# Performance work log

Measured on AMD Instinct MI355X. Metric: run time of the kernel, lower is better.

Reference implementation:

```python
import jax, jax.numpy as jnp
import numpy as np

# Dimensions (match init_kwargs / input_specs)
B, C, H, W = 16, 96, 224, 224
COUT = 96
PH, PW = 16, 16          # patch_size (== patch_stride, non-overlapping)
KH, KW = 3, 3            # patch_kernel and output_kernel
PAD = 1                  # padding
GH, GW = H // PH, W // PW
P = GH * GW              # num_patches = 196


def setup_inputs() -> dict:
    key = jax.random.key(0)
    k1, k2, k3 = jax.random.split(key, 3)
    x = jax.random.normal(k1, (B, C, H, W), dtype=jnp.float32)
    # kaiming-normal-ish init scales (fan_in over trailing dims, as torch does)
    pf = jax.random.normal(k2, (C, P, 1, KH, KW), dtype=jnp.float32) * np.float32(np.sqrt(2.0 / (P * KH * KW)))
    of = jax.random.normal(k3, (COUT, C, KH, KW), dtype=jnp.float32) * np.float32(np.sqrt(2.0 / (C * KH * KW)))
    return {"x": x, "patch_filters": pf, "output_filters": of}


def _self_conv2d(x, patch_filters):
    """Locally-connected per-patch depthwise conv.

    x: (B, C, H, W); patch_filters: (C, P, 1, KH, KW).
    Each of the P non-overlapping PHxPW patches of each channel is convolved
    with its own KHxKW kernel (padding=PAD, stride=1), then patches are
    reassembled into the full (B, C, H, W) map.
    """
    # (B, C, GH, PH, GW, PW) -> (B, C, GH, GW, PH, PW) -> (B, C*P, PH, PW)
    xp = x.reshape(B, C, GH, PH, GW, PW).transpose(0, 1, 2, 4, 3, 5).reshape(B, C * P, PH, PW)
    k = patch_filters.reshape(C * P, 1, KH, KW)
    y = jax.lax.conv_general_dilated(
        xp, k,
        window_strides=(1, 1),
        padding=[(PAD, PAD), (PAD, PAD)],
        feature_group_count=C * P,
        dimension_numbers=("NCHW", "OIHW", "NCHW"),
    )  # (B, C*P, PH, PW) since 3x3 conv with pad 1 preserves size
    return y.reshape(B, C, GH, GW, PH, PW).transpose(0, 1, 2, 4, 3, 5).reshape(B, C, H, W)


def reference(x, patch_filters, output_filters):
    # input already at (max_input_height, max_input_width) -> F.pad is a no-op
    sa = _self_conv2d(x, patch_filters)
    out = jax.lax.conv_general_dilated(
        sa, output_filters,
        window_strides=(1, 1),
        padding=[(PAD, PAD), (PAD, PAD)],
        dimension_numbers=("NCHW", "OIHW", "NCHW"),
    )  # (B, COUT, H, W)
    return jax.nn.gelu(out, approximate=False)  # torch nn.GELU() = exact erf gelu
```

## Files before the change

### kernel.cpp

```cpp
#include <hip/hip_runtime.h>
#include <hip/hip_bf16.h>

#define B_    16
#define C_    96
#define H_    224
#define W_    224
#define COUT_ 96
#define GH_   14
#define GW_   14
#define P_    196
#define HW_   (H_*W_)
#define NCH_  12

#define AS1 __attribute__((address_space(1)))
#define AS3 __attribute__((address_space(3)))

typedef __attribute__((ext_vector_type(8))) unsigned short ushort8;
typedef __attribute__((ext_vector_type(8))) short        short8;
typedef __attribute__((ext_vector_type(4))) float        f32x4;

__device__ __forceinline__ unsigned short f2bf(float f) {
    union { __hip_bfloat16 h; unsigned short u; } cv;
    cv.h = __float2bfloat16(f);
    return cv.u;
}

__global__ __launch_bounds__(256) void prep_ofb(const float* __restrict__ of,
                                                unsigned short* __restrict__ ofb,
                                                unsigned short* __restrict__ zp) {
    if (blockIdx.x == 0 && threadIdx.x < 128) zp[threadIdx.x] = 0;
    int idx = blockIdx.x * 256 + threadIdx.x;
    if (idx < 9 * 96 * 96) {
        int tap = idx / (96 * 96);
        int r   = idx % (96 * 96);
        int cout = r / 96, c = r % 96;
        ofb[idx] = f2bf(of[((size_t)cout * 96 + c) * 9 + tap]);
    }
}

__global__ __launch_bounds__(256) void sa_kernel(const float* __restrict__ x,
                                                 const float* __restrict__ pf,
                                                 unsigned short* __restrict__ sa) {
    int bid   = blockIdx.x;
    int patch = bid % P_;
    int b     = bid / P_;
    int gh = patch / GW_, gw = patch % GW_;
    int t  = threadIdx.x;
    int py = t >> 4, px = t & 15;
    int y  = gh * 16 + py, xx = gw * 16 + px;

    __shared__ float xs[2][8][256];

    const float* xp0 = x + (size_t)b * C_ * HW_ + (size_t)y * W_ + xx;

    float lf[8];
    #pragma unroll
    for (int ch = 0; ch < 8; ++ch) lf[ch] = xp0[(size_t)ch * HW_];

    for (int cc = 0; cc < NCH_; ++cc) {
        int buf = cc & 1;
        #pragma unroll
        for (int ch = 0; ch < 8; ++ch) xs[buf][ch][t] = lf[ch];
        __syncthreads();
        if (cc < NCH_ - 1) {
            #pragma unroll
            for (int ch = 0; ch < 8; ++ch)
                lf[ch] = xp0[(size_t)((cc + 1) * 8 + ch) * HW_];
        }

        ushort8 v;
        #pragma unroll
        for (int ch = 0; ch < 8; ++ch) {
            const float* wgt = pf + ((size_t)(cc * 8 + ch) * P_ + patch) * 9;
            float a = 0.f;
            #pragma unroll
            for (int dy = -1; dy <= 1; ++dy) {
                int yy = py + dy;
                if ((unsigned)yy < 16u) {
                    #pragma unroll
                    for (int dx = -1; dx <= 1; ++dx) {
                        int xq = px + dx;
                        if ((unsigned)xq < 16u)
                            a = fmaf(xs[buf][ch][yy * 16 + xq],
                                     wgt[(dy + 1) * 3 + (dx + 1)], a);
                    }
                }
            }
            v[ch] = f2bf(a);
        }
        *(ushort8*)&sa[(((size_t)(b * NCH_ + cc) * H_ + y) * W_ + xx) * 8] = v;
    }
}

__global__ __launch_bounds__(512, 4) void conv2_mfma(const unsigned short* __restrict__ sa,
                                                     const unsigned short* __restrict__ ofb,
                                                     const unsigned short* __restrict__ zp,
                                                     float* __restrict__ out) {
    int bid0 = blockIdx.x;
    int bid  = (bid0 % 8) * (3136 / 8) + bid0 / 8;
    int patch = bid % P_;
    int b     = bid / P_;
    int gh = patch / GW_, gw = patch % GW_;
    int y0 = gh * 16, x0 = gw * 16;

    int t = threadIdx.x;
    int w = t >> 6, l = t & 63;
    int wm = w & 3, wn = w >> 2;
    int mrow = l & 15, kgrp = l >> 4;

    __shared__ ushort8 at8[2][1536];

    auto STAGE = [&](int g) {
        int buf = g & 1;
        #pragma unroll
        for (int i = 0; i < 3; ++i) {
            int v = t + i * 512;
            const unsigned short* src = zp;
            if (v < 1296) {
                int ccl = v / 324, hpx = v - ccl * 324;
                int gy = y0 - 1 + hpx / 18, gx = x0 - 1 + hpx % 18;
                if ((unsigned)gy < (unsigned)H_ && (unsigned)gx < (unsigned)W_)
                    src = &sa[(((size_t)(b * NCH_ + g * 4 + ccl) * H_ + gy) * W_ + gx) * 8];
            }
            __builtin_amdgcn_global_load_lds((const AS1 unsigned int*)src,
                                             (AS3 unsigned int*)&at8[buf][v], 16, 0, 0);
        }
    };

    f32x4 acc[4][3];
    #pragma unroll
    for (int mi = 0; mi < 4; ++mi)
        #pragma unroll
        for (int ni = 0; ni < 3; ++ni)
            acc[mi][ni] = (f32x4)0.f;

    STAGE(0);
    #pragma unroll 1
    for (int g = 0; g < 3; ++g) {
        __syncthreads();
        if (g < 2) STAGE(g + 1);
        const unsigned short* atg = (const unsigned short*)at8[g & 1];

        #pragma unroll
        for (int tap = 0; tap < 9; ++tap) {
            int ky = tap / 3, kx = tap % 3;
            const unsigned short* bofs = ofb + tap * (96 * 96) + wn * 48 * 96
                                         + g * 32 + kgrp * 8;
            short8 bf[3];
            #pragma unroll
            for (int ni = 0; ni < 3; ++ni)
                bf[ni] = *(const short8*)&bofs[(ni * 16 + mrow) * 96];
            #pragma unroll
            for (int mi = 0; mi < 4; ++mi) {
                short8 af = *(const short8*)&atg[(kgrp * 324 + (wm * 4 + mi + ky) * 18
                                                 + kx + mrow) * 8];
                #pragma unroll
                for (int ni = 0; ni < 3; ++ni)
                    acc[mi][ni] = __builtin_amdgcn_mfma_f32_16x16x32_bf16(
                        af, bf[ni], acc[mi][ni], 0, 0, 0);
            }
        }
    }

    #pragma unroll
    for (int mi = 0; mi < 4; ++mi) {
        int gy = y0 + wm * 4 + mi;
        #pragma unroll
        for (int ni = 0; ni < 3; ++ni) {
            int cout = wn * 48 + ni * 16 + mrow;
            f32x4 gv;
            #pragma unroll
            for (int j = 0; j < 4; ++j) {
                float vv = acc[mi][ni][j];
                gv[j] = 0.5f * vv * (1.0f + erff(vv * 0.70710678118f));
            }
            *(f32x4*)&out[((size_t)b * COUT_ + cout) * HW_ + (size_t)gy * W_ +
                          x0 + kgrp * 4] = gv;
        }
    }
}

extern "C" void kernel_launch(void* const* d_in, const int* in_sizes, int n_in,
                              void* d_out, int out_size, void* d_ws, size_t ws_size,
                              hipStream_t stream) {
    const float* x  = (const float*)d_in[0];
    const float* pf = (const float*)d_in[1];
    const float* of = (const float*)d_in[2];
    float* out = (float*)d_out;

    unsigned short* sa  = (unsigned short*)d_ws;
    unsigned short* ofb = (unsigned short*)((char*)d_ws + 154140672);
    unsigned short* zp  = (unsigned short*)((char*)d_ws + 154306560);

    prep_ofb<<<324, 256, 0, stream>>>(of, ofb, zp);
    sa_kernel<<<B_ * P_, 256, 0, stream>>>(x, pf, sa);
    conv2_mfma<<<B_ * P_, 512, 0, stream>>>(sa, ofb, zp, out);
}
```

Baseline: 441.4 us.

## Use 4-wave blocks with full-COUT tiles and single-shot LDS staging in conv2

```diff
diff --git a/kernel.cpp b/kernel.cpp
--- a/kernel.cpp
+++ b/kernel.cpp
@@ -92,7 +92,7 @@
     }
 }
 
-__global__ __launch_bounds__(512, 4) void conv2_mfma(const unsigned short* __restrict__ sa,
+__global__ __launch_bounds__(256, 2) void conv2_mfma(const unsigned short* __restrict__ sa,
                                                      const unsigned short* __restrict__ ofb,
                                                      const unsigned short* __restrict__ zp,
                                                      float* __restrict__ out) {
@@ -105,69 +105,71 @@
 
     int t = threadIdx.x;
     int w = t >> 6, l = t & 63;
-    int wm = w & 3, wn = w >> 2;
     int mrow = l & 15, kgrp = l >> 4;
 
-    __shared__ ushort8 at8[2][1536];
-
-    auto STAGE = [&](int g) {
-        int buf = g & 1;
-        #pragma unroll
-        for (int i = 0; i < 3; ++i) {
-            int v = t + i * 512;
-            const unsigned short* src = zp;
-            if (v < 1296) {
-                int ccl = v / 324, hpx = v - ccl * 324;
-                int gy = y0 - 1 + hpx / 18, gx = x0 - 1 + hpx % 18;
-                if ((unsigned)gy < (unsigned)H_ && (unsigned)gx < (unsigned)W_)
-                    src = &sa[(((size_t)(b * NCH_ + g * 4 + ccl) * H_ + gy) * W_ + gx) * 8];
-            }
-            __builtin_amdgcn_global_load_lds((const AS1 unsigned int*)src,
-                                             (AS3 unsigned int*)&at8[buf][v], 16, 0, 0);
-        }
+    __shared__ ushort8 at8[4096];
+
+    #pragma unroll
+    for (int i = 0; i < 16; ++i) {
+        int v = t + i * 256;
+        const unsigned short* src = zp;
+        if (v < 3888) {
+            int ccl = v / 324, hpx = v - ccl * 324;
+            int gy = y0 - 1 + hpx / 18, gx = x0 - 1 + hpx % 18;
+            if ((unsigned)gy < (unsigned)H_ && (unsigned)gx < (unsigned)W_)
+                src = &sa[(((size_t)(b * NCH_ + ccl) * H_ + gy) * W_ + gx) * 8];
+        }
+        __builtin_amdgcn_global_load_lds((const AS1 unsigned int*)src,
+                                         (AS3 unsigned int*)&at8[v], 16, 0, 0);
+    }
+
+    f32x4 acc[4][6];
+    #pragma unroll
+    for (int mi = 0; mi < 4; ++mi)
+        #pragma unroll
+        for (int ni = 0; ni < 6; ++ni)
+            acc[mi][ni] = (f32x4)0.f;
+
+    __syncthreads();
+
+    const unsigned short* at = (const unsigned short*)at8;
+
+    short8 bfA[6], bfB[6];
+    auto LOADBF = [&](short8* dst, int T) {
+        int g = T / 9, tap = T % 9;
+        const unsigned short* bofs = ofb + tap * (96 * 96) + g * 32 + kgrp * 8;
+        #pragma unroll
+        for (int ni = 0; ni < 6; ++ni)
+            dst[ni] = *(const short8*)&bofs[(ni * 16 + mrow) * 96];
     };
 
-    f32x4 acc[4][3];
-    #pragma unroll
-    for (int mi = 0; mi < 4; ++mi)
-        #pragma unroll
-        for (int ni = 0; ni < 3; ++ni)
-            acc[mi][ni] = (f32x4)0.f;
-
-    STAGE(0);
-    #pragma unroll 1
-    for (int g = 0; g < 3; ++g) {
-        __syncthreads();
-        if (g < 2) STAGE(g + 1);
-        const unsigned short* atg = (const unsigned short*)at8[g & 1];
-
-        #pragma unroll
-        for (int tap = 0; tap < 9; ++tap) {
-            int ky = tap / 3, kx = tap % 3;
-            const unsigned short* bofs = ofb + tap * (96 * 96) + wn * 48 * 96
-                                         + g * 32 + kgrp * 8;
-            short8 bf[3];
-            #pragma unroll
-            for (int ni = 0; ni < 3; ++ni)
-                bf[ni] = *(const short8*)&bofs[(ni * 16 + mrow) * 96];
-            #pragma unroll
-            for (int mi = 0; mi < 4; ++mi) {
-                short8 af = *(const short8*)&atg[(kgrp * 324 + (wm * 4 + mi + ky) * 18
-                                                 + kx + mrow) * 8];
-                #pragma unroll
-                for (int ni = 0; ni < 3; ++ni)
-                    acc[mi][ni] = __builtin_amdgcn_mfma_f32_16x16x32_bf16(
-                        af, bf[ni], acc[mi][ni], 0, 0, 0);
-            }
+    LOADBF(bfA, 0);
+    #pragma unroll
+    for (int T = 0; T < 27; ++T) {
+        short8* cur = (T & 1) ? bfB : bfA;
+        short8* nxt = (T & 1) ? bfA : bfB;
+        if (T + 1 < 27) LOADBF(nxt, T + 1);
+
+        int g = T / 9, tap = T % 9;
+        int ky = tap / 3, kx = tap % 3;
+        #pragma unroll
+        for (int mi = 0; mi < 4; ++mi) {
+            short8 af = *(const short8*)&at[((g * 4 + kgrp) * 324
+                                            + (w * 4 + mi + ky) * 18
+                                            + kx + mrow) * 8];
+            #pragma unroll
+            for (int ni = 0; ni < 6; ++ni)
+                acc[mi][ni] = __builtin_amdgcn_mfma_f32_16x16x32_bf16(
+                    af, cur[ni], acc[mi][ni], 0, 0, 0);
         }
     }
 
     #pragma unroll
     for (int mi = 0; mi < 4; ++mi) {
-        int gy = y0 + wm * 4 + mi;
-        #pragma unroll
-        for (int ni = 0; ni < 3; ++ni) {
-            int cout = wn * 48 + ni * 16 + mrow;
+        int gy = y0 + w * 4 + mi;
+        #pragma unroll
+        for (int ni = 0; ni < 6; ++ni) {
+            int cout = ni * 16 + mrow;
             f32x4 gv;
             #pragma unroll
             for (int j = 0; j < 4; ++j) {
@@ -194,5 +196,5 @@
 
     prep_ofb<<<324, 256, 0, stream>>>(of, ofb, zp);
     sa_kernel<<<B_ * P_, 256, 0, stream>>>(x, pf, sa);
-    conv2_mfma<<<B_ * P_, 512, 0, stream>>>(sa, ofb, zp, out);
-}
+    conv2_mfma<<<B_ * P_, 256, 0, stream>>>(sa, ofb, zp, out);
+}
```

Result: faster. 404.4 us (-8.4%).
